# Kernel tuning notes

Measured on AMD Instinct MI355X. Metric: run time of the kernel, lower is better.

The kernel has to match this reference:

```python
import jax, jax.numpy as jnp
import numpy as np

TEMPERATURE = 0.1
KNN = 5
NEG = -1e30   # finite stand-in for -inf: identical softmax/threshold result, NaN-safe
EPS = -1e-08  # note: the original code really adds a NEGATIVE epsilon
MASK_VAL = -1.0


def setup_inputs() -> dict:
    key = jax.random.key(0)
    k1, k2, k3, k4 = jax.random.split(key, 4)
    n_img, max_r, n_cap, max_w, d = 128, 36, 128, 32, 512
    imgs = jax.random.normal(k1, (n_img, max_r, d), dtype=jnp.float32)
    caps = jax.random.normal(k2, (n_cap, max_w, d), dtype=jnp.float32)
    img_lens = jax.random.randint(k3, (n_img,), KNN + 1, max_r + 1, dtype=jnp.int32)
    cap_lens = jax.random.randint(k4, (n_cap,), 4, max_w + 1, dtype=jnp.int32)
    # guarantee lens.max() equals the static dims (torch slices to lens.max())
    img_lens = img_lens.at[0].set(max_r)
    cap_lens = cap_lens.at[0].set(max_w)
    return {"imgs": imgs, "caps": caps, "img_lens": img_lens, "cap_lens": cap_lens}


def reference(imgs, caps, img_lens, cap_lens):
    n_img, max_r, d = imgs.shape
    n_cap, max_w, _ = caps.shape
    knn = min(KNN, max_r)

    img_valid = jnp.arange(max_r)[None, :] < img_lens[:, None]   # [n_img, max_r]
    cap_valid = jnp.arange(max_w)[None, :] < cap_lens[:, None]   # [n_cap, max_w]
    imgs = jnp.where(img_valid[..., None], imgs, 0.0)
    caps = jnp.where(cap_valid[..., None], caps, 0.0)

    # fine-grained all-pairs similarities: [n_cap, n_img, max_w, max_r]
    sims = jnp.einsum('cwd,ird->ciwr', caps, imgs) / TEMPERATURE
    mask = cap_valid[:, None, :, None] & img_valid[None, :, None, :]
    sims = jnp.where(mask, sims, NEG)

    # top-KNN threshold along region axis (== sort()[..., max_r-KNN] in torch)
    kth = jax.lax.top_k(sims, knn)[0][..., -1:]
    sims = jnp.where(sims < kth, NEG, sims)

    attn = jax.nn.softmax(sims, axis=-1)
    attn = jnp.where(mask, attn, 0.0)

    att = jnp.einsum('ciwr,ird->ciwd', attn, imgs)                # attended regions
    num = jnp.einsum('ciwd,cwd->ciw', att, caps)
    den = jnp.linalg.norm(att, axis=-1) + EPS
    out = num / den                                               # [n_cap, n_img, max_w]
    out = jnp.where(cap_valid[:, None, :], out, MASK_VAL)
    return jnp.transpose(out, (1, 0, 2))                          # [n_img, n_cap, max_w]
```

## Files before the change

### kernel.cpp

```cpp
#include <hip/hip_runtime.h>
#include <cmath>

#define N_IMG 128
#define MAX_R 36
#define N_CAP 128
#define MAX_W 32
#define DIM   512
#define NEGV  -1e30f

typedef unsigned short u16;
typedef unsigned int   u32;
typedef unsigned char  u8;
typedef __attribute__((ext_vector_type(4))) int i32x4;

#define NI_ELEMS (N_IMG * MAX_R * DIM)
#define NC_ELEMS (N_CAP * MAX_W * DIM)
#define TOTAL4   ((NI_ELEMS + NC_ELEMS) / 4)

#define A_CHUNK 18432
#define B_CHUNK 16384
#define LDS_BYTES 53248
#define A1_OFF 18432
#define B_OFF  36864

__device__ __forceinline__ void gload_lds16(const void* g, void* l) {
    __builtin_amdgcn_global_load_lds(
        (const __attribute__((address_space(1))) void*)g,
        (__attribute__((address_space(3))) void*)l, 16, 0, 0);
}

__global__ __launch_bounds__(256) void convert_kernel(const float* __restrict__ imgs,
                                                      const float* __restrict__ caps,
                                                      u8* __restrict__ imgsT,
                                                      u8* __restrict__ capsT) {
    const size_t ni4 = NI_ELEMS / 4;
    const size_t p = (size_t)blockIdx.x * blockDim.x + threadIdx.x;
    if (p >= TOTAL4) return;
    const bool isImg = p < ni4;
    const float4 v = isImg ? ((const float4*)imgs)[p] : ((const float4*)caps)[p - ni4];
    const int q0 = (int)rintf(fminf(fmaxf(v.x * 4096.f, -32639.f), 32639.f));
    const int q1 = (int)rintf(fminf(fmaxf(v.y * 4096.f, -32639.f), 32639.f));
    const int q2 = (int)rintf(fminf(fmaxf(v.z * 4096.f, -32639.f), 32639.f));
    const int q3 = (int)rintf(fminf(fmaxf(v.w * 4096.f, -32639.f), 32639.f));
    const int h0 = (q0 + 128) >> 8, l0 = q0 - (h0 << 8);
    const int h1 = (q1 + 128) >> 8, l1 = q1 - (h1 << 8);
    const int h2 = (q2 + 128) >> 8, l2 = q2 - (h2 << 8);
    const int h3 = (q3 + 128) >> 8, l3 = q3 - (h3 << 8);
    const u32 hw = (u32)(h0 & 255) | ((u32)(h1 & 255) << 8) |
                   ((u32)(h2 & 255) << 16) | ((u32)(h3 & 255) << 24);
    const u32 lw = (u32)(l0 & 255) | ((u32)(l1 & 255) << 8) |
                   ((u32)(l2 & 255) << 16) | ((u32)(l3 & 255) << 24);
    if (isImg) {
        const int e = (int)(p * 4);
        const int imgRow = e >> 9, k = e & 511;
        const int g = imgRow / 144;
        const int rowT = imgRow - g * 144;
        const int kb = k >> 6, k6 = k & 63;
        const int blk = (k6 >> 4) ^ ((rowT >> 1) & 3);
        const size_t off = (size_t)(g * 8 + kb) * A_CHUNK + rowT * 64 + blk * 16 + (k6 & 15);
        *(u32*)(imgsT + off) = hw;
        *(u32*)(imgsT + off + 9216) = lw;
    } else {
        const int e = (int)((p - ni4) * 4);
        const int R = e >> 9, k = e & 511;
        const int cg = R >> 7, row = R & 127;
        const int kb = k >> 6, k6 = k & 63;
        const int blk = (k6 >> 4) ^ ((row >> 1) & 3);
        const size_t off = (size_t)(cg * 8 + kb) * B_CHUNK + row * 64 + blk * 16 + (k6 & 15);
        *(u32*)(capsT + off) = hw;
        *(u32*)(capsT + off + 8192) = lw;
    }
}

__global__ __launch_bounds__(256) void gram_i8_kernel(const u8* __restrict__ imgsT,
                                                      float* __restrict__ G) {
    const int i  = blockIdx.x;
    const int gg = i >> 2;
    const int m  = i & 3;
    const int t = threadIdx.x;
    const int wid = t >> 6;
    const int lane = t & 63;
    const int l15 = lane & 15;
    const int kq = lane >> 4;

    __shared__ __align__(16) u8 sT[2][2][3072];

    const u8* base = imgsT + (size_t)gg * 8 * A_CHUNK + m * 36 * 64;

    auto stage = [&](int kb, int buf) {
        const u8* hsrc = base + (size_t)kb * A_CHUNK;
        {
            const int u = t;
            if (u < 144) gload_lds16(hsrc + u * 16, &sT[buf][0][u * 16]);
            else if (u < 288) gload_lds16(hsrc + 9216 + (u - 144) * 16, &sT[buf][1][(u - 144) * 16]);
        }
        if (t < 32) {
            const int u = 112 + t;
            gload_lds16(hsrc + 9216 + u * 16, &sT[buf][1][u * 16]);
        }
    };

    i32x4 aH[3], aC[3], aL[3];
    #pragma unroll
    for (int mt = 0; mt < 3; ++mt) {
        aH[mt] = (i32x4){0,0,0,0};
        aC[mt] = (i32x4){0,0,0,0};
        aL[mt] = (i32x4){0,0,0,0};
    }

    stage(0, 0);
    __syncthreads();

    const int m18 = 18 * m;
    for (int kb = 0; kb < 8; ++kb) {
        const int buf = kb & 1;
        if (kb < 7) stage(kb + 1, buf ^ 1);
        if (wid < 3) {
            const int brow = wid * 16 + l15;
            const int bblk = kq ^ ((m18 + (brow >> 1)) & 3);
            const i32x4 bh = *(const i32x4*)&sT[buf][0][brow * 64 + bblk * 16];
            const i32x4 bl = *(const i32x4*)&sT[buf][1][brow * 64 + bblk * 16];
            #pragma unroll
            for (int mt = 0; mt < 3; ++mt) {
                const int arow = mt * 16 + l15;
                const int ablk = kq ^ ((m18 + (arow >> 1)) & 3);
                const i32x4 ah = *(const i32x4*)&sT[buf][0][arow * 64 + ablk * 16];
                const i32x4 al = *(const i32x4*)&sT[buf][1][arow * 64 + ablk * 16];
                aH[mt] = __builtin_amdgcn_mfma_i32_16x16x64_i8(ah, bh, aH[mt], 0, 0, 0);
                aC[mt] = __builtin_amdgcn_mfma_i32_16x16x64_i8(ah, bl, aC[mt], 0, 0, 0);
                aC[mt] = __builtin_amdgcn_mfma_i32_16x16x64_i8(al, bh, aC[mt], 0, 0, 0);
                aL[mt] = __builtin_amdgcn_mfma_i32_16x16x64_i8(al, bl, aL[mt], 0, 0, 0);
            }
        }
        __syncthreads();
    }

    if (wid < 3) {
        const int col = wid * 16 + l15;
        if (col < 36) {
            #pragma unroll
            for (int mt = 0; mt < 3; ++mt) {
                #pragma unroll
                for (int e = 0; e < 4; ++e) {
                    const int row = mt * 16 + kq * 4 + e;
                    if (row < 36) {
                        const float g = (float)aH[mt][e] * (1.f / 256.f)
                                      + (float)aC[mt][e] * (1.f / 65536.f)
                                      + (float)aL[mt][e] * (1.f / 16777216.f);
                        G[(size_t)i * 1296 + row * 36 + col] = g;
                    }
                }
            }
        }
    }
}

__global__ __launch_bounds__(256, 2) void vsc_mfma_kernel(const u8* __restrict__ imgsT,
                                const u8* __restrict__ capsT,
                                const int* __restrict__ img_lens,
                                const int* __restrict__ cap_lens,
                                const float* __restrict__ G,
                                float* __restrict__ out) {
    extern __shared__ __align__(16) char smem[];
    const int bid = blockIdx.x;
    const int xcd = bid & 7;
    const int r_  = bid >> 3;
    const int g   = (r_ >> 5) * 8 + xcd;
    const int cg  = r_ & 31;
    const int t = threadIdx.x;
    const int wid = t >> 6;
    const int lane = t & 63;
    const int l15 = lane & 15;
    const int kblk = lane >> 4;

    const u8* gA = imgsT + (size_t)g * 8 * A_CHUNK;
    const u8* gB = capsT + (size_t)cg * 8 * B_CHUNK;

    auto stage = [&](int kb, int abuf) {
        const u8* srcA = gA + (size_t)kb * A_CHUNK;
        char* dstA = smem + abuf * A1_OFF;
        {
            const int ub = wid * 288;
            #pragma unroll
            for (int jj = 0; jj < 4; ++jj) {
                const int u = ub + jj * 64 + lane;
                gload_lds16(srcA + u * 16, dstA + u * 16);
            }
            if (lane < 32) {
                const int u = ub + 256 + lane;
                gload_lds16(srcA + u * 16, dstA + u * 16);
            }
        }
        const u8* srcB = gB + (size_t)kb * B_CHUNK;
        char* dstB = smem + B_OFF;
        #pragma unroll
        for (int jj = 0; jj < 2; ++jj) {
            const int u = wid * 128 + jj * 64 + lane;
            gload_lds16(srcB + u * 16, dstB + u * 16);
            gload_lds16(srcB + 8192 + u * 16, dstB + 8192 + u * 16);
        }
    };

    i32x4 accH[9][2], accC[9][2];
    #pragma unroll
    for (int mt = 0; mt < 9; ++mt)
        #pragma unroll
        for (int nt = 0; nt < 2; ++nt) {
            accH[mt][nt] = (i32x4){0, 0, 0, 0};
            accC[mt][nt] = (i32x4){0, 0, 0, 0};
        }

    stage(0, 0);

    const int blk16 = (kblk ^ ((l15 >> 1) & 3)) << 4;
    const int baseA = l15 * 64 + blk16;
    const int baseB = (wid * 32 + l15) * 64 + blk16;

    for (int kb = 0; kb < 8; ++kb) {
        asm volatile("s_waitcnt vmcnt(0)" ::: "memory");
        __builtin_amdgcn_sched_barrier(0);
        __builtin_amdgcn_s_barrier();
        __builtin_amdgcn_sched_barrier(0);

        char* curA = smem + (size_t)(kb & 1) * A1_OFF;

        const i32x4 bh0 = *(const i32x4*)(smem + B_OFF + baseB);
        const i32x4 bl0 = *(const i32x4*)(smem + B_OFF + 8192 + baseB);
        const i32x4 bh1 = *(const i32x4*)(smem + B_OFF + baseB + 1024);
        const i32x4 bl1 = *(const i32x4*)(smem + B_OFF + 8192 + baseB + 1024);
        asm volatile("s_waitcnt lgkmcnt(0)" ::: "memory");
        __builtin_amdgcn_sched_barrier(0);

        if (kb < 7) stage(kb + 1, (kb + 1) & 1);

        __builtin_amdgcn_s_setprio(1);
        #pragma unroll
        for (int mt = 0; mt < 9; ++mt) {
            const i32x4 ah = *(const i32x4*)(curA + baseA + mt * 1024);
            const i32x4 al = *(const i32x4*)(curA + 9216 + baseA + mt * 1024);
            i32x4 lt0 = (i32x4){0, 0, 0, 0};
            i32x4 lt1 = (i32x4){0, 0, 0, 0};
            lt0 = __builtin_amdgcn_mfma_i32_16x16x64_i8(al, bl0, lt0, 0, 0, 0);
            lt1 = __builtin_amdgcn_mfma_i32_16x16x64_i8(al, bl1, lt1, 0, 0, 0);
            accH[mt][0] = __builtin_amdgcn_mfma_i32_16x16x64_i8(ah, bh0, accH[mt][0], 0, 0, 0);
            accH[mt][1] = __builtin_amdgcn_mfma_i32_16x16x64_i8(ah, bh1, accH[mt][1], 0, 0, 0);
            accC[mt][0] = __builtin_amdgcn_mfma_i32_16x16x64_i8(ah, bl0, accC[mt][0], 0, 0, 0);
            accC[mt][0] = __builtin_amdgcn_mfma_i32_16x16x64_i8(al, bh0, accC[mt][0], 0, 0, 0);
            accC[mt][1] = __builtin_amdgcn_mfma_i32_16x16x64_i8(ah, bl1, accC[mt][1], 0, 0, 0);
            accC[mt][1] = __builtin_amdgcn_mfma_i32_16x16x64_i8(al, bh1, accC[mt][1], 0, 0, 0);
            #pragma unroll
            for (int e = 0; e < 4; ++e) {
                accC[mt][0][e] += lt0[e] >> 8;
                accC[mt][1][e] += lt1[e] >> 8;
            }
        }
        __builtin_amdgcn_s_setprio(0);
    }

    __syncthreads();

    float* sG = (float*)smem;
    {
        const float4* src = (const float4*)(G + (size_t)g * 4 * 1296);
        for (int idx = t; idx < 1296; idx += 256)
            ((float4*)sG)[idx] = src[idx];
    }
    __syncthreads();

    int ilen_[4];
    #pragma unroll
    for (int j = 0; j < 4; ++j) ilen_[j] = img_lens[g * 4 + j];

    #pragma unroll
    for (int nt = 0; nt < 2; ++nt) {
        const int col = wid * 32 + nt * 16 + l15;
        const int c = cg * 4 + (col >> 5);
        const int w = col & 31;
        const int clen = cap_lens[c];
        #pragma unroll
        for (int j = 0; j < 4; ++j) {
            const int mtb = (36 * j) >> 4;
            const int ilenj = ilen_[j];
            float tv0 = NEGV, tv1 = NEGV, tv2 = NEGV, tv3 = NEGV, tv4 = NEGV;
            #pragma unroll
            for (int dm = 0; dm < 3; ++dm) {
                #pragma unroll
                for (int e = 0; e < 4; ++e) {
                    const int mt = mtb + dm;
                    const int r = mt * 16 + kblk * 4 + e;
                    const int rr = r - 36 * j;
                    const float sval = (float)accH[mt][nt][e] * (10.f / 256.f)
                                     + (float)accC[mt][nt][e] * (10.f / 65536.f);
                    float v = NEGV;
                    if ((unsigned)rr < (unsigned)ilenj)
                        v = __uint_as_float((__float_as_uint(sval) & ~63u) | (u32)rr);
                    const bool c0 = v > tv0, c1 = v > tv1, c2 = v > tv2, c3 = v > tv3, c4 = v > tv4;
                    const float n4 = c4 ? (c3 ? tv3 : v) : tv4;
                    const float n3 = c3 ? (c2 ? tv2 : v) : tv3;
                    const float n2 = c2 ? (c1 ? tv1 : v) : tv2;
                    const float n1 = c1 ? (c0 ? tv0 : v) : tv1;
                    const float n0 = c0 ? v : tv0;
                    tv0 = n0; tv1 = n1; tv2 = n2; tv3 = n3; tv4 = n4;
                }
            }
            float ta[5] = {tv0, tv1, tv2, tv3, tv4};
            #pragma unroll
            for (int st = 0; st < 2; ++st) {
                const int dx = 16 << st;
                float tb[5];
                #pragma unroll
                for (int s = 0; s < 5; ++s) tb[s] = __shfl_xor(ta[s], dx);
                float na[5];
                #pragma unroll
                for (int k = 0; k < 5; ++k) {
                    float best = fmaxf(ta[k], tb[k]);
                    #pragma unroll
                    for (int i2 = 1; i2 <= k; ++i2)
                        best = fmaxf(best, fminf(ta[i2 - 1], tb[k - i2]));
                    na[k] = best;
                }
                #pragma unroll
                for (int s = 0; s < 5; ++s) ta[s] = na[s];
            }
            const float m = ta[0];
            const float p0 = 1.f;
            const float p1 = __expf(ta[1] - m);
            const float p2 = __expf(ta[2] - m);
            const float p3 = __expf(ta[3] - m);
            const float p4 = __expf(ta[4] - m);
            const float sum = p0 + p1 + p2 + p3 + p4;
            const float num = p0 * ta[0] + p1 * ta[1] + p2 * ta[2] + p3 * ta[3] + p4 * ta[4];
            const int r0 = __float_as_uint(ta[0]) & 63;
            const int r1 = __float_as_uint(ta[1]) & 63;
            const int r2 = __float_as_uint(ta[2]) & 63;
            const int r3 = __float_as_uint(ta[3]) & 63;
            const int r4 = __float_as_uint(ta[4]) & 63;
            const float* gj = sG + j * 1296;
            const float pa = (kblk == 0) ? p0 : (kblk == 1) ? p1 : (kblk == 2) ? p2 : p3;
            const int   ra = (kblk == 0) ? r0 : (kblk == 1) ? r1 : (kblk == 2) ? r2 : r3;
            const float* grow = gj + ra * 36;
            float part = pa * (p0 * grow[r0] + p1 * grow[r1] + p2 * grow[r2]
                             + p3 * grow[r3] + p4 * grow[r4]);
            if (kblk == 0) {
                const float* grow4 = gj + r4 * 36;
                part += p4 * (p0 * grow4[r0] + p1 * grow4[r1] + p2 * grow4[r2]
                            + p3 * grow4[r3] + p4 * grow4[r4]);
            }
            part += __shfl_xor(part, 16);
            part += __shfl_xor(part, 32);
            if (kblk == j) {
                float result = -1.f;
                if (w < clen) {
                    const float inv = __builtin_amdgcn_rcpf(sum);
                    const float a_ = 0.1f * num * inv;
                    const float den = __builtin_amdgcn_sqrtf(part) * inv + (-1e-8f);
                    result = a_ * __builtin_amdgcn_rcpf(den);
                }
                out[((size_t)(g * 4 + j) * N_CAP + c) * MAX_W + w] = result;
            }
        }
    }
}

extern "C" void kernel_launch(void* const* d_in, const int* in_sizes, int n_in,
                              void* d_out, int out_size, void* d_ws, size_t ws_size,
                              hipStream_t stream) {
    const float* imgs     = (const float*)d_in[0];
    const float* caps     = (const float*)d_in[1];
    const int*   img_lens = (const int*)d_in[2];
    const int*   cap_lens = (const int*)d_in[3];
    float* out = (float*)d_out;

    float* G  = (float*)d_ws;
    u8* imgsT = (u8*)d_ws + 663552;
    u8* capsT = imgsT + (size_t)32 * 8 * A_CHUNK;

    hipFuncSetAttribute((const void*)vsc_mfma_kernel,
                        hipFuncAttributeMaxDynamicSharedMemorySize, LDS_BYTES);

    convert_kernel<<<4352, 256, 0, stream>>>(imgs, caps, imgsT, capsT);
    gram_i8_kernel<<<N_IMG, 256, 0, stream>>>(imgsT, G);
    vsc_mfma_kernel<<<1024, 256, LDS_BYTES, stream>>>(imgsT, capsT, img_lens, cap_lens, G, out);
}
```

Baseline: 76.52 us.

## Merge convert and gram kernels into one prep launch with in-LDS quantization

Folds the quantize/relayout kernel and the per-image Gram kernel into a single launch: the first blocks do the conversion while extra blocks re-read the float images directly, quantize into LDS and compute the Gram matrix. This removes one kernel launch and the dependency of the Gram step on the converted buffer, so both run concurrently. In exchange every block now requests 48KB of dynamic LDS, including the conversion blocks that never use it, which can limit how many of them fit per CU, and the image floats are read twice.

After: 78.39 us. 2.4% more time.

```diff
diff --git a/kernel.cpp b/kernel.cpp
--- a/kernel.cpp
+++ b/kernel.cpp
@@ -16,12 +16,15 @@
 #define NI_ELEMS (N_IMG * MAX_R * DIM)
 #define NC_ELEMS (N_CAP * MAX_W * DIM)
 #define TOTAL4   ((NI_ELEMS + NC_ELEMS) / 4)
+#define CONV_BLOCKS 4352
+#define PREP_BLOCKS (CONV_BLOCKS + N_IMG)
 
 #define A_CHUNK 18432
 #define B_CHUNK 16384
 #define LDS_BYTES 53248
 #define A1_OFF 18432
 #define B_OFF  36864
+#define PREP_LDS 49152
 
 __device__ __forceinline__ void gload_lds16(const void* g, void* l) {
     __builtin_amdgcn_global_load_lds(
@@ -29,15 +32,7 @@
         (__attribute__((address_space(3))) void*)l, 16, 0, 0);
 }
 
-__global__ __launch_bounds__(256) void convert_kernel(const float* __restrict__ imgs,
-                                                      const float* __restrict__ caps,
-                                                      u8* __restrict__ imgsT,
-                                                      u8* __restrict__ capsT) {
-    const size_t ni4 = NI_ELEMS / 4;
-    const size_t p = (size_t)blockIdx.x * blockDim.x + threadIdx.x;
-    if (p >= TOTAL4) return;
-    const bool isImg = p < ni4;
-    const float4 v = isImg ? ((const float4*)imgs)[p] : ((const float4*)caps)[p - ni4];
+__device__ __forceinline__ void quant4(const float4 v, u32& hw, u32& lw) {
     const int q0 = (int)rintf(fminf(fmaxf(v.x * 4096.f, -32639.f), 32639.f));
     const int q1 = (int)rintf(fminf(fmaxf(v.y * 4096.f, -32639.f), 32639.f));
     const int q2 = (int)rintf(fminf(fmaxf(v.z * 4096.f, -32639.f), 32639.f));
@@ -46,59 +41,75 @@
     const int h1 = (q1 + 128) >> 8, l1 = q1 - (h1 << 8);
     const int h2 = (q2 + 128) >> 8, l2 = q2 - (h2 << 8);
     const int h3 = (q3 + 128) >> 8, l3 = q3 - (h3 << 8);
-    const u32 hw = (u32)(h0 & 255) | ((u32)(h1 & 255) << 8) |
-                   ((u32)(h2 & 255) << 16) | ((u32)(h3 & 255) << 24);
-    const u32 lw = (u32)(l0 & 255) | ((u32)(l1 & 255) << 8) |
-                   ((u32)(l2 & 255) << 16) | ((u32)(l3 & 255) << 24);
-    if (isImg) {
-        const int e = (int)(p * 4);
-        const int imgRow = e >> 9, k = e & 511;
-        const int g = imgRow / 144;
-        const int rowT = imgRow - g * 144;
-        const int kb = k >> 6, k6 = k & 63;
-        const int blk = (k6 >> 4) ^ ((rowT >> 1) & 3);
-        const size_t off = (size_t)(g * 8 + kb) * A_CHUNK + rowT * 64 + blk * 16 + (k6 & 15);
-        *(u32*)(imgsT + off) = hw;
-        *(u32*)(imgsT + off + 9216) = lw;
-    } else {
-        const int e = (int)((p - ni4) * 4);
-        const int R = e >> 9, k = e & 511;
-        const int cg = R >> 7, row = R & 127;
-        const int kb = k >> 6, k6 = k & 63;
-        const int blk = (k6 >> 4) ^ ((row >> 1) & 3);
-        const size_t off = (size_t)(cg * 8 + kb) * B_CHUNK + row * 64 + blk * 16 + (k6 & 15);
-        *(u32*)(capsT + off) = hw;
-        *(u32*)(capsT + off + 8192) = lw;
-    }
-}
-
-__global__ __launch_bounds__(256) void gram_i8_kernel(const u8* __restrict__ imgsT,
-                                                      float* __restrict__ G) {
-    const int i  = blockIdx.x;
-    const int gg = i >> 2;
-    const int m  = i & 3;
+    hw = (u32)(h0 & 255) | ((u32)(h1 & 255) << 8) |
+         ((u32)(h2 & 255) << 16) | ((u32)(h3 & 255) << 24);
+    lw = (u32)(l0 & 255) | ((u32)(l1 & 255) << 8) |
+         ((u32)(l2 & 255) << 16) | ((u32)(l3 & 255) << 24);
+}
+
+__global__ __launch_bounds__(256) void prep_kernel(const float* __restrict__ imgs,
+                                                   const float* __restrict__ caps,
+                                                   u8* __restrict__ imgsT,
+                                                   u8* __restrict__ capsT,
+                                                   float* __restrict__ G) {
+    extern __shared__ __align__(16) char smem[];
+    const int bid = blockIdx.x;
     const int t = threadIdx.x;
+
+    if (bid < CONV_BLOCKS) {
+        const size_t ni4 = NI_ELEMS / 4;
+        const size_t p = (size_t)bid * 256 + t;
+        if (p >= TOTAL4) return;
+        const bool isImg = p < ni4;
+        const float4 v = isImg ? ((const float4*)imgs)[p] : ((const float4*)caps)[p - ni4];
+        u32 hw, lw;
+        quant4(v, hw, lw);
+        if (isImg) {
+            const int e = (int)(p * 4);
+            const int imgRow = e >> 9, k = e & 511;
+            const int g = imgRow / 144;
+            const int rowT = imgRow - g * 144;
+            const int kb = k >> 6, k6 = k & 63;
+            const int blk = (k6 >> 4) ^ ((rowT >> 1) & 3);
+            const size_t off = (size_t)(g * 8 + kb) * A_CHUNK + rowT * 64 + blk * 16 + (k6 & 15);
+            *(u32*)(imgsT + off) = hw;
+            *(u32*)(imgsT + off + 9216) = lw;
+        } else {
+            const int e = (int)((p - ni4) * 4);
+            const int R = e >> 9, k = e & 511;
+            const int cg = R >> 7, row = R & 127;
+            const int kb = k >> 6, k6 = k & 63;
+            const int blk = (k6 >> 4) ^ ((row >> 1) & 3);
+            const size_t off = (size_t)(cg * 8 + kb) * B_CHUNK + row * 64 + blk * 16 + (k6 & 15);
+            *(u32*)(capsT + off) = hw;
+            *(u32*)(capsT + off + 8192) = lw;
+        }
+        return;
+    }
+
+    const int i = bid - CONV_BLOCKS;
     const int wid = t >> 6;
     const int lane = t & 63;
     const int l15 = lane & 15;
     const int kq = lane >> 4;
 
-    __shared__ __align__(16) u8 sT[2][2][3072];
-
-    const u8* base = imgsT + (size_t)gg * 8 * A_CHUNK + m * 36 * 64;
-
-    auto stage = [&](int kb, int buf) {
-        const u8* hsrc = base + (size_t)kb * A_CHUNK;
-        {
-            const int u = t;
-            if (u < 144) gload_lds16(hsrc + u * 16, &sT[buf][0][u * 16]);
-            else if (u < 288) gload_lds16(hsrc + 9216 + (u - 144) * 16, &sT[buf][1][(u - 144) * 16]);
-        }
-        if (t < 32) {
-            const int u = 112 + t;
-            gload_lds16(hsrc + 9216 + u * 16, &sT[buf][1][u * 16]);
-        }
-    };
+    u8* sH = (u8*)smem;
+    u8* sL = (u8*)smem + 24576;
+
+    const float* base = imgs + (size_t)i * MAX_R * DIM;
+    for (int idx = t; idx < 4608; idx += 256) {
+        const int e = idx * 4;
+        const int row = e >> 9, k = e & 511;
+        const float4 v = *(const float4*)(base + e);
+        u32 hw, lw;
+        quant4(v, hw, lw);
+        const int kb = k >> 6, k6 = k & 63;
+        const int blk = (k6 >> 4) ^ ((row >> 1) & 3);
+        const int off = kb * 3072 + row * 64 + blk * 16 + (k6 & 15);
+        *(u32*)(sH + off) = hw;
+        *(u32*)(sL + off) = lw;
+    }
+    __syncthreads();
 
     i32x4 aH[3], aC[3], aL[3];
     #pragma unroll
@@ -108,34 +119,26 @@
         aL[mt] = (i32x4){0,0,0,0};
     }
 
-    stage(0, 0);
-    __syncthreads();
-
-    const int m18 = 18 * m;
-    for (int kb = 0; kb < 8; ++kb) {
-        const int buf = kb & 1;
-        if (kb < 7) stage(kb + 1, buf ^ 1);
-        if (wid < 3) {
+    if (wid < 3) {
+        for (int kb = 0; kb < 8; ++kb) {
+            const u8* hb = sH + kb * 3072;
+            const u8* lb = sL + kb * 3072;
             const int brow = wid * 16 + l15;
-            const int bblk = kq ^ ((m18 + (brow >> 1)) & 3);
-            const i32x4 bh = *(const i32x4*)&sT[buf][0][brow * 64 + bblk * 16];
-            const i32x4 bl = *(const i32x4*)&sT[buf][1][brow * 64 + bblk * 16];
+            const int bblk = kq ^ ((brow >> 1) & 3);
+            const i32x4 bh = *(const i32x4*)(hb + brow * 64 + bblk * 16);
+            const i32x4 bl = *(const i32x4*)(lb + brow * 64 + bblk * 16);
             #pragma unroll
             for (int mt = 0; mt < 3; ++mt) {
                 const int arow = mt * 16 + l15;
-                const int ablk = kq ^ ((m18 + (arow >> 1)) & 3);
-                const i32x4 ah = *(const i32x4*)&sT[buf][0][arow * 64 + ablk * 16];
-                const i32x4 al = *(const i32x4*)&sT[buf][1][arow * 64 + ablk * 16];
+                const int ablk = kq ^ ((arow >> 1) & 3);
+                const i32x4 ah = *(const i32x4*)(hb + arow * 64 + ablk * 16);
+                const i32x4 al = *(const i32x4*)(lb + arow * 64 + ablk * 16);
                 aH[mt] = __builtin_amdgcn_mfma_i32_16x16x64_i8(ah, bh, aH[mt], 0, 0, 0);
                 aC[mt] = __builtin_amdgcn_mfma_i32_16x16x64_i8(ah, bl, aC[mt], 0, 0, 0);
                 aC[mt] = __builtin_amdgcn_mfma_i32_16x16x64_i8(al, bh, aC[mt], 0, 0, 0);
                 aL[mt] = __builtin_amdgcn_mfma_i32_16x16x64_i8(al, bl, aL[mt], 0, 0, 0);
             }
         }
-        __syncthreads();
-    }
-
-    if (wid < 3) {
         const int col = wid * 16 + l15;
         if (col < 36) {
             #pragma unroll
@@ -375,10 +378,11 @@
     u8* imgsT = (u8*)d_ws + 663552;
     u8* capsT = imgsT + (size_t)32 * 8 * A_CHUNK;
 
+    hipFuncSetAttribute((const void*)prep_kernel,
+                        hipFuncAttributeMaxDynamicSharedMemorySize, PREP_LDS);
     hipFuncSetAttribute((const void*)vsc_mfma_kernel,
                         hipFuncAttributeMaxDynamicSharedMemorySize, LDS_BYTES);
 
-    convert_kernel<<<4352, 256, 0, stream>>>(imgs, caps, imgsT, capsT);
-    gram_i8_kernel<<<N_IMG, 256, 0, stream>>>(imgsT, G);
+    prep_kernel<<<PREP_BLOCKS, 256, PREP_LDS, stream>>>(imgs, caps, imgsT, capsT, G);
     vsc_mfma_kernel<<<1024, 256, LDS_BYTES, stream>>>(imgsT, capsT, img_lens, cap_lens, G, out);
 }
```
